# Optimization experiments

Measured on AMD Instinct MI355X. Metric: run time of the kernel, lower is better.

## Reference

```python
import jax, jax.numpy as jnp
import numpy as np

B, S, D_IN, D_OUT = 4, 2048, 1024, 1024

def setup_inputs() -> dict:
    key = jax.random.key(0)
    k1, k2, k3, k4, k5, k6 = jax.random.split(key, 6)
    return {
        "inputs_for_keys": jax.random.normal(k1, (B, S, D_IN), dtype=jnp.float32),
        "inputs_for_values": jax.random.normal(k2, (B, S, D_IN), dtype=jnp.float32),
        "inputs_for_queries": jax.random.normal(k3, (B, S, D_IN), dtype=jnp.float32),
        "WK": jax.random.truncated_normal(k4, -2.0, 2.0, (D_IN, D_OUT), dtype=jnp.float32) * 0.1,
        "WV": jax.random.truncated_normal(k5, -2.0, 2.0, (D_IN, D_OUT), dtype=jnp.float32) * 0.1,
        "WQ": jax.random.truncated_normal(k6, -2.0, 2.0, (D_IN, D_OUT), dtype=jnp.float32) * 0.1,
    }

def reference(inputs_for_keys, inputs_for_values, inputs_for_queries, WK, WV, WQ):
    # projections: [B,S,D_in] @ [D_in,D_out] -> [B,S,D_out]
    K = jnp.einsum('bsd,de->bse', inputs_for_keys, WK)
    V = jnp.einsum('bsd,de->bse', inputs_for_values, WV)
    Q = jnp.einsum('bsd,de->bse', inputs_for_queries, WQ)
    # scores: [B,S,S]. NOTE: original TF code scales by sqrt(K.shape[1]) = sqrt(seq_len),
    # not sqrt(head_dim) — reproduce that faithfully.
    scale = jnp.sqrt(jnp.float32(K.shape[1]))
    scores = jnp.einsum('bqe,bke->bqk', Q, K) / scale
    attn = jax.nn.softmax(scores, axis=-1)
    return jnp.einsum('bqk,bke->bqe', attn, V)
```

## Files before the change

kernel.cpp:

```cpp
#include <hip/hip_runtime.h>
#include <hip/hip_bf16.h>


typedef __attribute__((ext_vector_type(4))) float    f32x4;
typedef __attribute__((ext_vector_type(8))) _Float16 f16x8;
typedef __attribute__((ext_vector_type(4))) _Float16 f16x4;

constexpr size_t MiB = 1u << 20;
constexpr size_t MK  = (size_t)8192 * 1024;
constexpr size_t WSZ = (size_t)1024 * 1024;

__device__ __forceinline__ void gload_lds16(const void* g, void* l) {
  __builtin_amdgcn_global_load_lds(
      (const __attribute__((address_space(1))) unsigned int*)g,
      (__attribute__((address_space(3))) unsigned int*)l, 16, 0, 0);
}

#define MFMA16(a, b, c) __builtin_amdgcn_mfma_f32_16x16x32_f16(a, b, c, 0, 0, 0)

__device__ __forceinline__ void swz_block(int& bx, int& by, int& bz) {
  unsigned gx = gridDim.x, gy = gridDim.y;
  unsigned flat = blockIdx.x + gx * (blockIdx.y + gy * blockIdx.z);
  unsigned total = gx * gy * gridDim.z;
  unsigned cpx = total >> 3;
  unsigned s = (flat & 7) * cpx + (flat >> 3);
  bx = s % gx; s /= gx; by = s % gy; bz = s / gy;
}

__global__ __launch_bounds__(256) void convert_x(
    const float* __restrict__ x0, const float* __restrict__ x1,
    const float* __restrict__ x2, _Float16* __restrict__ XF)
{
  const int z = blockIdx.z;
  const float* x = z == 0 ? x0 : (z == 1 ? x1 : x2);
  size_t i = ((size_t)blockIdx.x * 256 + threadIdx.x) * 4;
  float4 v = *(const float4*)(x + i);
  f16x4 h = {(_Float16)v.x, (_Float16)v.y, (_Float16)v.z, (_Float16)v.w};
  *(f16x4*)(XF + (size_t)z * MK + i) = h;
}

__global__ __launch_bounds__(256) void transpose_conv_w(
    const float* __restrict__ w0, const float* __restrict__ w1,
    const float* __restrict__ w2, _Float16* __restrict__ WT)
{
  const int z = blockIdx.z;
  const float* W = z == 0 ? w0 : (z == 1 ? w1 : w2);
  _Float16* o = WT + (size_t)z * WSZ;
  __shared__ float tile[32][33];
  const int bx = blockIdx.x * 32;
  const int by = blockIdx.y * 32;
  const int tx = threadIdx.x & 31, ty = threadIdx.x >> 5;
  #pragma unroll
  for (int r = 0; r < 32; r += 8)
    tile[ty + r][tx] = W[(size_t)(by + ty + r) * 1024 + bx + tx];
  __syncthreads();
  #pragma unroll
  for (int r = 0; r < 32; r += 8)
    o[(size_t)(bx + ty + r) * 1024 + by + tx] = (_Float16)tile[tx][ty + r];
}

__global__ __launch_bounds__(256) void transpose_v(
    const _Float16* __restrict__ V, _Float16* __restrict__ Vt)
{
  const _Float16* v = V + (size_t)blockIdx.z * 2048 * 1024;
  _Float16* o = Vt + (size_t)blockIdx.z * 1024 * 2048;
  __shared__ _Float16 tile[32][33];
  const int bx = blockIdx.x * 32;
  const int by = blockIdx.y * 32;
  const int tx = threadIdx.x & 31, ty = threadIdx.x >> 5;
  #pragma unroll
  for (int r = 0; r < 32; r += 8)
    tile[ty + r][tx] = v[(size_t)(by + ty + r) * 1024 + bx + tx];
  __syncthreads();
  #pragma unroll
  for (int r = 0; r < 32; r += 8)
    o[(size_t)(bx + ty + r) * 2048 + by + tx] = tile[tx][ty + r];
}

template <int MODE>
__global__ __launch_bounds__(512, 4) void gemmO(
    const _Float16* __restrict__ At, size_t sA,
    const _Float16* __restrict__ Bt, size_t sB,
    void* __restrict__ Cv, size_t sCz,
    int N, int K, float scale)
{
  extern __shared__ char lds[];
  int bx, by, bz;
  swz_block(bx, by, bz);
  const _Float16* A = At + (size_t)bz * sA;
  const _Float16* B = Bt + (size_t)bz * sB;

  const int gm0 = by * 256, gn0 = bx * 128;
  const int tid = threadIdx.x;
  const int lane = tid & 63, wave = tid >> 6;
  const int wm = (wave >> 1) * 64;
  const int wn = (wave & 1) * 64;
  const int fr = lane & 15, fq = lane >> 4;
  const int nkt = K >> 5;

  const int clog = ((tid & 3) ^ ((tid >> 3) & 3)) * 8;
  const _Float16* srcA = A + (size_t)(gm0 + (tid >> 2)) * K + clog;
  const _Float16* srcB = B + (size_t)(gn0 + (tid >> 2)) * K + clog;
  char* const dst0 = lds + tid * 16;

  auto STG = [&](int tile) {
    const int off = tile * 32;
    char* d = dst0 + (tile % 3) * 24576;
    gload_lds16(srcA + off,                   d);
    gload_lds16(srcA + off + (size_t)128 * K, d + 8192);
    gload_lds16(srcB + off,                   d + 16384);
  };

  const int pc  = (fq ^ ((fr >> 1) & 3)) * 16;
  const int arb = (wm + fr) * 64 + pc;
  const int brb = 16384 + (wn + fr) * 64 + pc;

  f32x4 acc[4][4] = {};
  f16x8 af[4], bfr[4];

  STG(0);
  if (nkt > 1) {
    STG(1);
    asm volatile("s_waitcnt vmcnt(3)" ::: "memory");
  } else {
    asm volatile("s_waitcnt vmcnt(0)" ::: "memory");
  }
  __builtin_amdgcn_s_barrier();
  __builtin_amdgcn_sched_barrier(0);

  for (int t = 0; t < nkt; ++t) {
    const char* buf = lds + (t % 3) * 24576;
    const bool st2 = (t + 2) < nkt;

    if (st2) STG(t + 2);

    #pragma unroll
    for (int mi = 0; mi < 4; ++mi)
      af[mi] = *(const f16x8*)(buf + arb + mi * 1024);
    #pragma unroll
    for (int ni = 0; ni < 4; ++ni)
      bfr[ni] = *(const f16x8*)(buf + brb + ni * 1024);

    __builtin_amdgcn_s_setprio(1);
    #pragma unroll
    for (int mi = 0; mi < 4; ++mi)
      #pragma unroll
      for (int ni = 0; ni < 4; ++ni)
        acc[mi][ni] = MFMA16(af[mi], bfr[ni], acc[mi][ni]);
    __builtin_amdgcn_s_setprio(0);

    if (st2)               asm volatile("s_waitcnt vmcnt(3)" ::: "memory");
    else if (t + 1 < nkt)  asm volatile("s_waitcnt vmcnt(0)" ::: "memory");
    __builtin_amdgcn_s_barrier();
    __builtin_amdgcn_sched_barrier(0);
  }

  const int erow = gm0 + wm + fq * 4;
  const int ecol = gn0 + wn + fr;
  #pragma unroll
  for (int m = 0; m < 4; ++m)
    #pragma unroll
    for (int n = 0; n < 4; ++n) {
      size_t base = (size_t)(erow + m * 16) * N + (ecol + n * 16);
      #pragma unroll
      for (int r = 0; r < 4; ++r) {
        float v = acc[m][n][r];
        if constexpr (MODE == 0)
          ((float*)Cv + (size_t)bz * sCz)[base + (size_t)r * N] = v * scale;
        else if constexpr (MODE == 1)
          ((_Float16*)Cv + (size_t)bz * sCz)[base + (size_t)r * N] = (_Float16)v;
        else
          ((_Float16*)Cv + (size_t)bz * sCz)[base + (size_t)r * N] =
              (_Float16)(v * scale);
      }
    }
}

__global__ __launch_bounds__(256) void softmax_rows(
    const _Float16* __restrict__ S, _Float16* __restrict__ P)
{
  const int w = threadIdx.x >> 6, lane = threadIdx.x & 63;
  const size_t row = (size_t)blockIdx.x * 4 + w;
  const _Float16* sr = S + row * 2048;

  f16x8 v[4];
  #pragma unroll
  for (int c = 0; c < 4; ++c)
    v[c] = *(const f16x8*)(sr + c * 512 + lane * 8);

  float m = -1e30f;
  #pragma unroll
  for (int c = 0; c < 4; ++c)
    #pragma unroll
    for (int j = 0; j < 8; ++j) m = fmaxf(m, (float)v[c][j]);
  #pragma unroll
  for (int o = 32; o >= 1; o >>= 1) m = fmaxf(m, __shfl_xor(m, o));

  float e[4][8];
  float s = 0.f;
  #pragma unroll
  for (int c = 0; c < 4; ++c)
    #pragma unroll
    for (int j = 0; j < 8; ++j) {
      e[c][j] = __expf((float)v[c][j] - m);
      s += e[c][j];
    }
  #pragma unroll
  for (int o = 32; o >= 1; o >>= 1) s += __shfl_xor(s, o);

  const float inv = 1.0f / s;
  _Float16* pr = P + row * 2048;
  #pragma unroll
  for (int c = 0; c < 4; ++c) {
    f16x8 p;
    #pragma unroll
    for (int j = 0; j < 8; ++j) p[j] = (_Float16)(e[c][j] * inv);
    *(f16x8*)(pr + c * 512 + lane * 8) = p;
  }
}

extern "C" void kernel_launch(void* const* d_in, const int* in_sizes, int n_in,
                              void* d_out, int out_size, void* d_ws, size_t ws_size,
                              hipStream_t stream)
{
  const float* Xk = (const float*)d_in[0];
  const float* Xv = (const float*)d_in[1];
  const float* Xq = (const float*)d_in[2];
  const float* WK = (const float*)d_in[3];
  const float* WV = (const float*)d_in[4];
  const float* WQ = (const float*)d_in[5];
  float* out = (float*)d_out;
  char* ws = (char*)d_ws;

  _Float16* XF   = (_Float16*)(ws);
  _Float16* WT   = (_Float16*)(ws + 48 * MiB);
  _Float16* PROJ = (_Float16*)(ws + 54 * MiB);
  _Float16* VT   = (_Float16*)(ws + 102 * MiB);
  _Float16* SC   = (_Float16*)(ws + 118 * MiB);
  _Float16* P    = (_Float16*)(ws);

  _Float16* Kp = PROJ;
  _Float16* Vp = PROJ + MK;
  _Float16* Qp = PROJ + 2 * MK;

  auto* fP  = gemmO<1>;
  auto* fSC = gemmO<2>;
  auto* fPV = gemmO<0>;
  (void)hipFuncSetAttribute((const void*)fP,  hipFuncAttributeMaxDynamicSharedMemorySize, 73728);
  (void)hipFuncSetAttribute((const void*)fSC, hipFuncAttributeMaxDynamicSharedMemorySize, 73728);
  (void)hipFuncSetAttribute((const void*)fPV, hipFuncAttributeMaxDynamicSharedMemorySize, 73728);

  convert_x<<<dim3(8192, 1, 3), 256, 0, stream>>>(Xk, Xv, Xq, XF);
  transpose_conv_w<<<dim3(32, 32, 3), 256, 0, stream>>>(WK, WV, WQ, WT);
  gemmO<1><<<dim3(8, 32, 3), 512, 73728, stream>>>(
      XF, MK, WT, WSZ, PROJ, MK, 1024, 1024, 1.0f);
  transpose_v<<<dim3(32, 64, 4), 256, 0, stream>>>(Vp, VT);
  gemmO<2><<<dim3(16, 8, 4), 512, 73728, stream>>>(
      Qp, (size_t)2048 * 1024, Kp, (size_t)2048 * 1024,
      SC, (size_t)2048 * 2048, 2048, 1024, 0.022097086912079608f);
  softmax_rows<<<dim3(2048), 256, 0, stream>>>(SC, P);
  gemmO<0><<<dim3(8, 8, 4), 512, 73728, stream>>>(
      P, (size_t)2048 * 2048, VT, (size_t)1024 * 2048,
      out, (size_t)2048 * 1024, 1024, 2048, 1.0f);
}
```

Measured before the change: 199.8 us.

## Compute V projection transposed directly and merge prep kernels into one launch

Computes V^T directly as WV^T·Xv^T with a separate GEMM that writes a [1024, 8192] layout, which removes the transpose_v kernel and its extra read and write of V. The GEMM now takes explicit leading dimensions so strided batch views can be used. It also fuses the input conversion and weight transpose into a single prep kernel to save a launch. The V GEMM now runs as a separate launch of 256 blocks, which may use the device less fully than the batched K/Q launch.

```diff
diff --git a/kernel.cpp b/kernel.cpp
--- a/kernel.cpp
+++ b/kernel.cpp
@@ -27,68 +27,53 @@
   bx = s % gx; s /= gx; by = s % gy; bz = s / gy;
 }
 
-__global__ __launch_bounds__(256) void convert_x(
+__global__ __launch_bounds__(256) void prep(
     const float* __restrict__ x0, const float* __restrict__ x1,
-    const float* __restrict__ x2, _Float16* __restrict__ XF)
-{
-  const int z = blockIdx.z;
-  const float* x = z == 0 ? x0 : (z == 1 ? x1 : x2);
-  size_t i = ((size_t)blockIdx.x * 256 + threadIdx.x) * 4;
-  float4 v = *(const float4*)(x + i);
-  f16x4 h = {(_Float16)v.x, (_Float16)v.y, (_Float16)v.z, (_Float16)v.w};
-  *(f16x4*)(XF + (size_t)z * MK + i) = h;
-}
-
-__global__ __launch_bounds__(256) void transpose_conv_w(
+    const float* __restrict__ x2, _Float16* __restrict__ XF,
     const float* __restrict__ w0, const float* __restrict__ w1,
     const float* __restrict__ w2, _Float16* __restrict__ WT)
 {
-  const int z = blockIdx.z;
-  const float* W = z == 0 ? w0 : (z == 1 ? w1 : w2);
-  _Float16* o = WT + (size_t)z * WSZ;
-  __shared__ float tile[32][33];
-  const int bx = blockIdx.x * 32;
-  const int by = blockIdx.y * 32;
-  const int tx = threadIdx.x & 31, ty = threadIdx.x >> 5;
-  #pragma unroll
-  for (int r = 0; r < 32; r += 8)
-    tile[ty + r][tx] = W[(size_t)(by + ty + r) * 1024 + bx + tx];
-  __syncthreads();
-  #pragma unroll
-  for (int r = 0; r < 32; r += 8)
-    o[(size_t)(bx + ty + r) * 1024 + by + tx] = (_Float16)tile[tx][ty + r];
-}
-
-__global__ __launch_bounds__(256) void transpose_v(
-    const _Float16* __restrict__ V, _Float16* __restrict__ Vt)
-{
-  const _Float16* v = V + (size_t)blockIdx.z * 2048 * 1024;
-  _Float16* o = Vt + (size_t)blockIdx.z * 1024 * 2048;
-  __shared__ _Float16 tile[32][33];
-  const int bx = blockIdx.x * 32;
-  const int by = blockIdx.y * 32;
-  const int tx = threadIdx.x & 31, ty = threadIdx.x >> 5;
-  #pragma unroll
-  for (int r = 0; r < 32; r += 8)
-    tile[ty + r][tx] = v[(size_t)(by + ty + r) * 1024 + bx + tx];
-  __syncthreads();
-  #pragma unroll
-  for (int r = 0; r < 32; r += 8)
-    o[(size_t)(bx + ty + r) * 2048 + by + tx] = tile[tx][ty + r];
+  const unsigned id = blockIdx.x;
+  if (id < 24576) {
+    const int z = id >> 13;
+    const unsigned blk = id & 8191;
+    const float* x = z == 0 ? x0 : (z == 1 ? x1 : x2);
+    size_t i = ((size_t)blk * 256 + threadIdx.x) * 4;
+    float4 v = *(const float4*)(x + i);
+    f16x4 h = {(_Float16)v.x, (_Float16)v.y, (_Float16)v.z, (_Float16)v.w};
+    *(f16x4*)(XF + (size_t)z * MK + i) = h;
+  } else {
+    const unsigned rem = id - 24576;
+    const int z = rem >> 10;
+    const unsigned blk = rem & 1023;
+    const float* W = z == 0 ? w0 : (z == 1 ? w1 : w2);
+    _Float16* o = WT + (size_t)z * WSZ;
+    __shared__ float tile[32][33];
+    const int bx = (blk & 31) * 32;
+    const int by = (blk >> 5) * 32;
+    const int tx = threadIdx.x & 31, ty = threadIdx.x >> 5;
+    #pragma unroll
+    for (int r = 0; r < 32; r += 8)
+      tile[ty + r][tx] = W[(size_t)(by + ty + r) * 1024 + bx + tx];
+    __syncthreads();
+    #pragma unroll
+    for (int r = 0; r < 32; r += 8)
+      o[(size_t)(bx + ty + r) * 1024 + by + tx] = (_Float16)tile[tx][ty + r];
+  }
 }
 
 template <int MODE>
 __global__ __launch_bounds__(512, 4) void gemmO(
-    const _Float16* __restrict__ At, size_t sA,
-    const _Float16* __restrict__ Bt, size_t sB,
-    void* __restrict__ Cv, size_t sCz,
-    int N, int K, float scale)
+    const _Float16* __restrict__ At, size_t sAz, int lda,
+    const _Float16* __restrict__ Bt, size_t sBz, int ldb,
+    void* __restrict__ Cv, size_t sCz, int ldc,
+    int K, float scale)
 {
   extern __shared__ char lds[];
   int bx, by, bz;
   swz_block(bx, by, bz);
-  const _Float16* A = At + (size_t)bz * sA;
-  const _Float16* B = Bt + (size_t)bz * sB;
+  const _Float16* A = At + (size_t)bz * sAz;
+  const _Float16* B = Bt + (size_t)bz * sBz;
 
   const int gm0 = by * 256, gn0 = bx * 128;
   const int tid = threadIdx.x;
@@ -99,16 +84,16 @@
   const int nkt = K >> 5;
 
   const int clog = ((tid & 3) ^ ((tid >> 3) & 3)) * 8;
-  const _Float16* srcA = A + (size_t)(gm0 + (tid >> 2)) * K + clog;
-  const _Float16* srcB = B + (size_t)(gn0 + (tid >> 2)) * K + clog;
+  const _Float16* srcA = A + (size_t)(gm0 + (tid >> 2)) * lda + clog;
+  const _Float16* srcB = B + (size_t)(gn0 + (tid >> 2)) * ldb + clog;
   char* const dst0 = lds + tid * 16;
 
   auto STG = [&](int tile) {
     const int off = tile * 32;
     char* d = dst0 + (tile % 3) * 24576;
-    gload_lds16(srcA + off,                   d);
-    gload_lds16(srcA + off + (size_t)128 * K, d + 8192);
-    gload_lds16(srcB + off,                   d + 16384);
+    gload_lds16(srcA + off,                     d);
+    gload_lds16(srcA + off + (size_t)128 * lda, d + 8192);
+    gload_lds16(srcB + off,                     d + 16384);
   };
 
   const int pc  = (fq ^ ((fr >> 1) & 3)) * 16;
@@ -161,17 +146,17 @@
   for (int m = 0; m < 4; ++m)
     #pragma unroll
     for (int n = 0; n < 4; ++n) {
-      size_t base = (size_t)(erow + m * 16) * N + (ecol + n * 16);
+      size_t base = (size_t)(erow + m * 16) * ldc + (ecol + n * 16);
       #pragma unroll
       for (int r = 0; r < 4; ++r) {
         float v = acc[m][n][r];
+        size_t idx = base + (size_t)r * ldc;
         if constexpr (MODE == 0)
-          ((float*)Cv + (size_t)bz * sCz)[base + (size_t)r * N] = v * scale;
+          ((float*)Cv + (size_t)bz * sCz)[idx] = v * scale;
         else if constexpr (MODE == 1)
-          ((_Float16*)Cv + (size_t)bz * sCz)[base + (size_t)r * N] = (_Float16)v;
+          ((_Float16*)Cv + (size_t)bz * sCz)[idx] = (_Float16)v;
         else
-          ((_Float16*)Cv + (size_t)bz * sCz)[base + (size_t)r * N] =
-              (_Float16)(v * scale);
+          ((_Float16*)Cv + (size_t)bz * sCz)[idx] = (_Float16)(v * scale);
       }
     }
 }
@@ -235,31 +220,32 @@
   _Float16* XF   = (_Float16*)(ws);
   _Float16* WT   = (_Float16*)(ws + 48 * MiB);
   _Float16* PROJ = (_Float16*)(ws + 54 * MiB);
-  _Float16* VT   = (_Float16*)(ws + 102 * MiB);
-  _Float16* SC   = (_Float16*)(ws + 118 * MiB);
+  _Float16* VTf  = (_Float16*)(ws + 86 * MiB);
+  _Float16* SC   = (_Float16*)(ws + 102 * MiB);
   _Float16* P    = (_Float16*)(ws);
 
   _Float16* Kp = PROJ;
-  _Float16* Vp = PROJ + MK;
-  _Float16* Qp = PROJ + 2 * MK;
-
-  auto* fP  = gemmO<1>;
-  auto* fSC = gemmO<2>;
-  auto* fPV = gemmO<0>;
-  (void)hipFuncSetAttribute((const void*)fP,  hipFuncAttributeMaxDynamicSharedMemorySize, 73728);
-  (void)hipFuncSetAttribute((const void*)fSC, hipFuncAttributeMaxDynamicSharedMemorySize, 73728);
-  (void)hipFuncSetAttribute((const void*)fPV, hipFuncAttributeMaxDynamicSharedMemorySize, 73728);
-
-  convert_x<<<dim3(8192, 1, 3), 256, 0, stream>>>(Xk, Xv, Xq, XF);
-  transpose_conv_w<<<dim3(32, 32, 3), 256, 0, stream>>>(WK, WV, WQ, WT);
-  gemmO<1><<<dim3(8, 32, 3), 512, 73728, stream>>>(
-      XF, MK, WT, WSZ, PROJ, MK, 1024, 1024, 1.0f);
-  transpose_v<<<dim3(32, 64, 4), 256, 0, stream>>>(Vp, VT);
+  _Float16* Qp = PROJ + MK;
+
+  auto* f1 = gemmO<1>;
+  auto* f2 = gemmO<2>;
+  auto* f0 = gemmO<0>;
+  (void)hipFuncSetAttribute((const void*)f1, hipFuncAttributeMaxDynamicSharedMemorySize, 73728);
+  (void)hipFuncSetAttribute((const void*)f2, hipFuncAttributeMaxDynamicSharedMemorySize, 73728);
+  (void)hipFuncSetAttribute((const void*)f0, hipFuncAttributeMaxDynamicSharedMemorySize, 73728);
+
+  prep<<<dim3(27648), 256, 0, stream>>>(Xk, Xv, Xq, XF, WK, WV, WQ, WT);
+  gemmO<1><<<dim3(8, 32, 2), 512, 73728, stream>>>(
+      XF, 2 * MK, 1024, WT, 2 * WSZ, 1024,
+      PROJ, MK, 1024, 1024, 1.0f);
+  gemmO<1><<<dim3(64, 4, 1), 512, 73728, stream>>>(
+      WT + WSZ, 0, 1024, XF + MK, 0, 1024,
+      VTf, 0, 8192, 1024, 1.0f);
   gemmO<2><<<dim3(16, 8, 4), 512, 73728, stream>>>(
-      Qp, (size_t)2048 * 1024, Kp, (size_t)2048 * 1024,
+      Qp, (size_t)2048 * 1024, 1024, Kp, (size_t)2048 * 1024, 1024,
       SC, (size_t)2048 * 2048, 2048, 1024, 0.022097086912079608f);
   softmax_rows<<<dim3(2048), 256, 0, stream>>>(SC, P);
   gemmO<0><<<dim3(8, 8, 4), 512, 73728, stream>>>(
-      P, (size_t)2048 * 2048, VT, (size_t)1024 * 2048,
+      P, (size_t)2048 * 2048, 2048, VTf, 2048, 8192,
       out, (size_t)2048 * 1024, 1024, 2048, 1.0f);
 }
```

New measurement: 195.3 us. 2.2% less time.
